# Optimization experiments

Hardware: AMD Instinct MI355X
Metric: run time of the kernel (lower is better)

## Reference

```python
import jax, jax.numpy as jnp
import numpy as np

B, H, W, C = 32, 56, 56, 256
WS = 7            # window size (hard-coded 49=7*7 in original topk modules)
NH = 8            # num heads
HD = C // NH      # head dim = 32
KCH = HD // 2     # channel top-k = 16
KSPT = 28         # spatial top-k
N = WS * WS       # 49 tokens per window
SCALE = HD ** -0.5
MLP_H = 4 * C

def _rel_index(ws):
    coords = np.stack(np.meshgrid(np.arange(ws), np.arange(ws), indexing='ij')).reshape(2, -1)
    rc = (coords[:, :, None] - coords[:, None, :]).transpose(1, 2, 0).astype(np.int64)
    rc[:, :, 0] += ws - 1
    rc[:, :, 1] += ws - 1
    rc[:, :, 0] *= 2 * ws - 1
    return jnp.asarray(rc.sum(-1))  # (N, N)

REL_IDX = _rel_index(WS)

def setup_inputs():
    key = jax.random.key(0)
    ks = jax.random.split(key, 10)
    p = lambda k, shp: jax.random.normal(k, shp, jnp.float32) * 0.02
    return dict(
        x=jax.random.normal(ks[0], (B, H * W, C), jnp.float32),
        norm1_g=jnp.ones((C,), jnp.float32), norm1_b=jnp.zeros((C,), jnp.float32),
        wq=p(ks[1], (C, C)), bq=jnp.zeros((C,), jnp.float32),
        wk=p(ks[2], (C // 2, C // 2)), bk=jnp.zeros((C // 2,), jnp.float32),
        wv=p(ks[3], (C, C)), bv=jnp.zeros((C,), jnp.float32),
        wproj=p(ks[4], (C, C)), bproj=jnp.zeros((C,), jnp.float32),
        wch=p(ks[5], (2 * HD, HD)), bch=jnp.zeros((HD,), jnp.float32),
        rpb_table=p(ks[6], ((2 * WS - 1) ** 2, NH)),
        norm2_g=jnp.ones((C,), jnp.float32), norm2_b=jnp.zeros((C,), jnp.float32),
        w1=p(ks[7], (C, MLP_H)), b1=jnp.zeros((MLP_H,), jnp.float32),
        w2=p(ks[8], (MLP_H, C)), b2=jnp.zeros((C,), jnp.float32),
    )

def _ln(x, g, b):
    mu = x.mean(-1, keepdims=True)
    var = x.var(-1, keepdims=True)
    return (x - mu) / jnp.sqrt(var + 1e-5) * g + b

def reference(x, norm1_g, norm1_b, wq, bq, wk, bk, wv, bv, wproj, bproj,
              wch, bch, rpb_table, norm2_g, norm2_b, w1, b1, w2, b2):
    shortcut = x
    xn = _ln(x, norm1_g, norm1_b).reshape(B, H, W, C)
    # window partition -> (Bw, N, C)
    xw = xn.reshape(B, H // WS, WS, W // WS, WS, C).transpose(0, 1, 3, 2, 4, 5).reshape(-1, N, C)
    Bw = xw.shape[0]
    q = xw @ wq + bq                                                    # (Bw, N, C)
    qh = q.reshape(Bw, N, NH, HD).transpose(0, 2, 1, 3).reshape(Bw * NH, N, HD)
    # ---- channel top-k (ChannelTopk) ----
    feat = jnp.concatenate([qh.mean(1), qh.max(1)], axis=-1)            # (Bn, 2*HD)
    score = jax.nn.softmax(jax.nn.gelu(feat @ wch + bch, approximate=False), axis=1)
    _, cidx = jax.lax.top_k(score, KCH)
    cidx = jnp.sort(cidx, axis=-1)                                      # sorted channel indices
    qcha = jnp.take_along_axis(qh, cidx[:, None, :], axis=2)            # (Bn, N, KCH)
    qcha1 = qcha.reshape(Bw, NH, N, KCH).transpose(0, 2, 1, 3).reshape(Bw, N, C // 2)
    k = qcha1 @ wk + bk                                                 # (Bw, N, C/2)
    # ---- relative position bias ----
    rpb = rpb_table[REL_IDX.reshape(-1)].reshape(N, N, NH).transpose(2, 0, 1)  # (NH, N, N)
    # ---- spatial top-k (SptialTopk) ----
    _, sidx = jax.lax.top_k(qh.mean(-1), KSPT)
    sidx = jnp.sort(sidx, axis=-1)                                      # (Bn, KSPT)
    qal = jnp.take_along_axis(qcha, sidx[:, :, None], axis=1)           # (Bn, KSPT, KCH)
    vsel = jnp.take_along_axis(qh, sidx[:, :, None], axis=1)            # (Bn, KSPT, HD)
    sidx_h = sidx.reshape(Bw, NH, KSPT)
    yal = jnp.take_along_axis(
        jnp.broadcast_to(rpb[None], (Bw, NH, N, N)),
        jnp.broadcast_to(sidx_h[:, :, None, :], (Bw, NH, N, KSPT)), axis=-1)  # (Bw, NH, N, KSPT)
    # ---- attention ----
    v = vsel.reshape(Bw, NH, KSPT, HD).transpose(0, 2, 1, 3).reshape(Bw, KSPT, C)
    v = (v @ wv + bv).reshape(Bw, KSPT, NH, HD).transpose(0, 2, 1, 3)   # (Bw, NH, KSPT, HD)
    qspt = (qal * SCALE).reshape(Bw, NH, KSPT, KCH)
    kh = k.reshape(Bw, N, NH, KCH).transpose(0, 2, 1, 3)                # (Bw, NH, N, KCH)
    attn = jnp.einsum('bnqc,bnkc->bnqk', kh, qspt) + yal                # (Bw, NH, N, KSPT)
    gate = jax.nn.sigmoid(attn.mean(-1))                                # (Bw, NH, N)
    attn = jax.nn.softmax(attn, axis=-1)
    o = jnp.einsum('bnqk,bnkd->bnqd', attn, v) * gate[..., None]        # (Bw, NH, N, HD)
    o = o.transpose(0, 2, 1, 3).reshape(Bw, N, C)
    o = o @ wproj + bproj
    # window reverse -> (B, L, C)
    xr = o.reshape(B, H // WS, W // WS, WS, WS, C).transpose(0, 1, 3, 2, 4, 5).reshape(B, H * W, C)
    x = shortcut + xr
    h = jax.nn.gelu(_ln(x, norm2_g, norm2_b) @ w1 + b1, approximate=False)
    return x + h @ w2 + b2
```

## Files before the change

### kernel.cpp

```cpp
#include <hip/hip_runtime.h>
#include <hip/hip_bf16.h>
#include <cmath>

#define CC 256
#define WSZ 7
#define WWD_ 56
#define NHD 8
#define HDIM 32
#define KCHN 16
#define KSP 28
#define NTOK 49
#define NWIN 2048
#define NBH 16384
#define LL 3136
#define MTOK 100352
#define MLPH 1024
#define SCALE_Q 0.17677669529663689f

typedef float floatx4 __attribute__((ext_vector_type(4)));
typedef __bf16 bf16x8_t __attribute__((ext_vector_type(8)));

__device__ __forceinline__ float gelu_f(float x) {
    return 0.5f * x * (1.0f + erff(x * 0.7071067811865475f));
}

__device__ __forceinline__ void lds_dma16(const void* g, void* l) {
    __builtin_amdgcn_global_load_lds((__attribute__((address_space(1))) void*)(void*)g,
                                     (__attribute__((address_space(3))) void*)l, 16, 0, 0);
}

__global__ __launch_bounds__(64) void ln_stats_k(const float* __restrict__ x,
                                                 float* __restrict__ mu,
                                                 float* __restrict__ rs) {
    int row = blockIdx.x;
    int lane = threadIdx.x;
    float4 v = reinterpret_cast<const float4*>(x + (size_t)row * CC)[lane];
    float s = v.x + v.y + v.z + v.w;
    float s2 = v.x * v.x + v.y * v.y + v.z * v.z + v.w * v.w;
#pragma unroll
    for (int off = 32; off > 0; off >>= 1) {
        s += __shfl_down(s, off);
        s2 += __shfl_down(s2, off);
    }
    if (lane == 0) {
        float m = s * (1.0f / CC);
        float var = s2 * (1.0f / CC) - m * m;
        mu[row] = m;
        rs[row] = rsqrtf(var + 1e-5f);
    }
}

struct GP {
    const float* W;
    const float* bias;
    float* C;
    int N, K;
    const float* x;
    const float* mu;
    const float* rs;
    const float* g;
    const float* be;
};

__global__ __launch_bounds__(256, 6) void gemm_q_k(GP p) {
    __shared__ __align__(16) float As[16][68];
    __shared__ __align__(16) float Bs[16][128];
    const int bm = blockIdx.x * 64;
    const int bn = blockIdx.y * 128;
    const int t = threadIdx.x;
    const int tx = t & 31;
    const int ty = t >> 5;
    const int w = t >> 6;

    const int ar = t >> 2;
    const int ak = (t & 3) * 4;

    const int r = bm + ar;
    int bwi = r / NTOK, n = r - bwi * NTOK;
    int b = bwi >> 6, rem = bwi & 63;
    int hw = rem >> 3, ww = rem & 7;
    int i0 = n / WSZ, j0 = n - i0 * WSZ;
    size_t grow = (size_t)b * LL + (size_t)(hw * WSZ + i0) * WWD_ + (ww * WSZ + j0);
    const float m = p.mu[grow], rsg = p.rs[grow];
    const float* xrow = p.x + grow * CC + ak;
    const float* gl = p.g + ak;
    const float* bl = p.be + ak;

    float acc[8][4] = {};

    for (int k0 = 0; k0 < CC; k0 += 16) {
        {
            float4 xv = *reinterpret_cast<const float4*>(xrow + k0);
            float4 gv = *reinterpret_cast<const float4*>(gl + k0);
            float4 bv = *reinterpret_cast<const float4*>(bl + k0);
            As[ak + 0][ar] = (xv.x - m) * rsg * gv.x + bv.x;
            As[ak + 1][ar] = (xv.y - m) * rsg * gv.y + bv.y;
            As[ak + 2][ar] = (xv.z - m) * rsg * gv.z + bv.z;
            As[ak + 3][ar] = (xv.w - m) * rsg * gv.w + bv.w;
        }
#pragma unroll
        for (int j = 0; j < 2; ++j) {
            const int c = j * 256 + t;
            const float* gp = p.W + (size_t)(k0 + (c >> 5)) * CC + bn + (c & 31) * 4;
            lds_dma16(gp, (char*)&Bs[0][0] + j * 4096 + w * 1024);
        }
        __syncthreads();
#pragma unroll
        for (int kk = 0; kk < 16; ++kk) {
            float a[8], bb[4];
            *(float4*)&a[0] = *(const float4*)&As[kk][ty * 8];
            *(float4*)&a[4] = *(const float4*)&As[kk][ty * 8 + 4];
            *(float4*)&bb[0] = *(const float4*)&Bs[kk][tx * 4];
#pragma unroll
            for (int i = 0; i < 8; ++i)
#pragma unroll
                for (int j = 0; j < 4; ++j) acc[i][j] = fmaf(a[i], bb[j], acc[i][j]);
        }
        __syncthreads();
    }

    float bj[4];
#pragma unroll
    for (int j = 0; j < 4; ++j) bj[j] = p.bias[bn + tx * 4 + j];
#pragma unroll
    for (int i = 0; i < 8; ++i) {
        const int row = bm + ty * 8 + i;
        float4 o = {acc[i][0] + bj[0], acc[i][1] + bj[1], acc[i][2] + bj[2], acc[i][3] + bj[3]};
        *reinterpret_cast<float4*>(p.C + (size_t)row * CC + bn + tx * 4) = o;
    }
}

struct MG {
    const __hip_bfloat16* A;
    const __hip_bfloat16* B;
    const float* bias;
    int N, K;
    float* Cf;
    __hip_bfloat16* Cb;
    const float* resid;
    int row0;
};

template <int EPI>
__global__ __launch_bounds__(256) void mgemm_k(MG p) {
    __shared__ __align__(16) __hip_bfloat16 As[2][128 * 32];
    __shared__ __align__(16) __hip_bfloat16 Bs[2][128 * 32];
    const int bm = blockIdx.x * 128;
    const int bn = blockIdx.y * 128;
    const int t = threadIdx.x;
    const int lane = t & 63;
    const int w = t >> 6;
    const int wm = (w & 1) * 64;
    const int wn = (w >> 1) * 64;
    const int fr = lane & 15;
    const int fk = (lane >> 4) * 8;

    const int m0 = t >> 2, m1 = (t + 256) >> 2;
    const int kc = (t & 3) * 8;
    const __hip_bfloat16* a0 = p.A + (size_t)(bm + m0) * p.K + kc;
    const __hip_bfloat16* a1 = p.A + (size_t)(bm + m1) * p.K + kc;
    const __hip_bfloat16* b0 = p.B + (size_t)(bn + m0) * p.K + kc;
    const __hip_bfloat16* b1 = p.B + (size_t)(bn + m1) * p.K + kc;

    auto stage = [&](int buf, int k0) {
        lds_dma16(a0 + k0, &As[buf][w * 512]);
        lds_dma16(a1 + k0, &As[buf][2048 + w * 512]);
        lds_dma16(b0 + k0, &Bs[buf][w * 512]);
        lds_dma16(b1 + k0, &Bs[buf][2048 + w * 512]);
    };

    floatx4 acc[4][4] = {};

    stage(0, 0);
    __syncthreads();
    int cur = 0;
    for (int k0 = 0; k0 < p.K; k0 += 32) {
        if (k0 + 32 < p.K) stage(cur ^ 1, k0 + 32);
        bf16x8_t af[4], bf[4];
#pragma unroll
        for (int i = 0; i < 4; ++i)
            af[i] = *(const bf16x8_t*)&As[cur][(wm + i * 16 + fr) * 32 + fk];
#pragma unroll
        for (int j = 0; j < 4; ++j)
            bf[j] = *(const bf16x8_t*)&Bs[cur][(wn + j * 16 + fr) * 32 + fk];
#pragma unroll
        for (int i = 0; i < 4; ++i)
#pragma unroll
            for (int j = 0; j < 4; ++j)
                acc[i][j] = __builtin_amdgcn_mfma_f32_16x16x32_bf16(af[i], bf[j], acc[i][j], 0, 0, 0);
        __syncthreads();
        cur ^= 1;
    }

    float bj[4];
#pragma unroll
    for (int j = 0; j < 4; ++j) bj[j] = p.bias[bn + wn + j * 16 + fr];
#pragma unroll
    for (int i = 0; i < 4; ++i) {
#pragma unroll
        for (int r = 0; r < 4; ++r) {
            const int m = bm + wm + i * 16 + (lane >> 4) * 4 + r;
#pragma unroll
            for (int j = 0; j < 4; ++j) {
                const int n = bn + wn + j * 16 + fr;
                float v = acc[i][j][r] + bj[j];
                if constexpr (EPI == 0) {
                    p.Cb[(size_t)m * p.N + n] = __float2bfloat16(v);
                } else if constexpr (EPI == 1) {
                    int bwi = m / NTOK, nn = m - bwi * NTOK;
                    int b = bwi >> 6, rem = bwi & 63;
                    int hw = rem >> 3, wwp = rem & 7;
                    int ii = nn / WSZ, jj = nn - ii * WSZ;
                    size_t oidx = ((size_t)b * LL + (size_t)(hw * WSZ + ii) * WWD_ + (wwp * WSZ + jj)) * CC + n;
                    p.Cf[oidx] = v + p.resid[oidx];
                } else if constexpr (EPI == 2) {
                    p.Cb[(size_t)m * p.N + n] = __float2bfloat16(gelu_f(v));
                } else {
                    size_t gr = (size_t)(m + p.row0);
                    p.Cf[gr * p.N + n] = v + p.resid[gr * p.N + n];
                }
            }
        }
    }
}

__global__ __launch_bounds__(256) void wt_k(const float* __restrict__ W,
                                            __hip_bfloat16* __restrict__ Wt, int K, int N) {
    int g = blockIdx.x * 256 + threadIdx.x;
    if (g >= K * N) return;
    int n = g / K, kk = g - n * K;
    Wt[g] = __float2bfloat16(W[(size_t)kk * N + n]);
}

__global__ __launch_bounds__(64) void topk_k(const float* __restrict__ q,
                                             const float* __restrict__ wch,
                                             const float* __restrict__ bch,
                                             short* __restrict__ cidx,
                                             short* __restrict__ sidx) {
    int bnh = blockIdx.x;
    int bwi = bnh >> 3, h = bnh & 7;
    int lane = threadIdx.x;
    __shared__ float tile[NTOK][HDIM + 1];
    __shared__ float feat[2 * HDIM];
    __shared__ float score[HDIM];
    __shared__ float rowm[NTOK];
    const float* qbase = q + ((size_t)bwi * NTOK) * CC + h * HDIM;
    for (int idx = lane; idx < NTOK * HDIM; idx += 64) {
        int n = idx >> 5, d = idx & 31;
        tile[n][d] = qbase[(size_t)n * CC + d];
    }
    __syncthreads();
    if (lane < HDIM) {
        float s = 0.f, mx = -INFINITY;
        for (int n = 0; n < NTOK; ++n) {
            float v = tile[n][lane];
            s += v;
            mx = fmaxf(mx, v);
        }
        feat[lane] = s * (1.0f / NTOK);
        feat[HDIM + lane] = mx;
    }
    if (lane < NTOK) {
        float s = 0.f;
        for (int d = 0; d < HDIM; ++d) s += tile[lane][d];
        rowm[lane] = s;
    }
    __syncthreads();
    if (lane < HDIM) {
        float s = bch[lane];
        for (int j = 0; j < 2 * HDIM; ++j) s += feat[j] * wch[j * HDIM + lane];
        score[lane] = gelu_f(s);
    }
    __syncthreads();
    {
        bool sel = false;
        if (lane < HDIM) {
            float sv = score[lane];
            int rank = 0;
            for (int j = 0; j < HDIM; ++j) {
                float oj = score[j];
                rank += (oj > sv) || (oj == sv && j < lane);
            }
            sel = rank < KCHN;
        }
        unsigned long long m = __ballot(sel);
        if (sel) {
            int pos = __popcll(m & ((1ull << lane) - 1ull));
            cidx[(size_t)bnh * KCHN + pos] = (short)lane;
        }
    }
    {
        bool sel = false;
        if (lane < NTOK) {
            float sv = rowm[lane];
            int rank = 0;
            for (int j = 0; j < NTOK; ++j) {
                float oj = rowm[j];
                rank += (oj > sv) || (oj == sv && j < lane);
            }
            sel = rank < KSP;
        }
        unsigned long long m = __ballot(sel);
        if (sel) {
            int pos = __popcll(m & ((1ull << lane) - 1ull));
            sidx[(size_t)bnh * KSP + pos] = (short)lane;
        }
    }
}

__global__ __launch_bounds__(256) void gather_ch_k(const float* __restrict__ q,
                                                   const short* __restrict__ cidx,
                                                   __hip_bfloat16* __restrict__ ak) {
    int g = blockIdx.x * 256 + threadIdx.x;
    int r = g >> 7, kk = g & 127;
    int bwi = r / NTOK;
    int hp = kk >> 4, c = kk & 15;
    int ci = cidx[((size_t)(bwi * NHD + hp)) * KCHN + c];
    ak[g] = __float2bfloat16(q[(size_t)r * CC + hp * HDIM + ci]);
}

__global__ __launch_bounds__(256) void gather_sp_k(const float* __restrict__ q,
                                                   const short* __restrict__ sidx,
                                                   __hip_bfloat16* __restrict__ av) {
    int g = blockIdx.x * 256 + threadIdx.x;
    int rr = g >> 8, c = g & 255;
    int bwi = rr / KSP, s = rr - bwi * KSP;
    int tok = sidx[((size_t)(bwi * NHD + (c >> 5))) * KSP + s];
    av[g] = __float2bfloat16(q[((size_t)(bwi * NTOK + tok)) * CC + c]);
}

__global__ __launch_bounds__(512) void attn_k(const float* __restrict__ q,
                                              const __hip_bfloat16* __restrict__ kb,
                                              const __hip_bfloat16* __restrict__ vb,
                                              const short* __restrict__ cidx,
                                              const short* __restrict__ sidx,
                                              const float* __restrict__ rpb,
                                              __hip_bfloat16* __restrict__ ob) {
    const int bwi = blockIdx.x;
    const int tid = threadIdx.x;
    const int h = tid >> 6;
    const int lane = tid & 63;
    __shared__ __hip_bfloat16 kh_s[NTOK][132];
    __shared__ float v_s[KSP][256];
    __shared__ float qs_s[NHD][KSP][KCHN];
    __shared__ int sidx_s[NHD][KSP];
    __shared__ int cidx_s[NHD][KCHN];

    if (tid < NHD * KSP) {
        sidx_s[tid / KSP][tid % KSP] = sidx[(size_t)bwi * NHD * KSP + tid];
    } else if (tid < NHD * KSP + NHD * KCHN) {
        int u = tid - NHD * KSP;
        cidx_s[u / KCHN][u % KCHN] = cidx[(size_t)bwi * NHD * KCHN + u];
    }
    {
        const __hip_bfloat16* kbase = kb + (size_t)bwi * NTOK * (NHD * KCHN);
        for (int ch = tid; ch < NTOK * 16; ch += 512) {
            int n = ch >> 4, c8 = (ch & 15) * 8;
            uint4 u = *(const uint4*)(kbase + n * 128 + c8);
            uint2* dst = (uint2*)&kh_s[n][c8];
            dst[0] = make_uint2(u.x, u.y);
            dst[1] = make_uint2(u.z, u.w);
        }
    }
    {
        const __hip_bfloat16* vbase = vb + (size_t)bwi * KSP * CC;
        for (int ch = tid; ch < KSP * 32; ch += 512) {
            int n = ch >> 5, c8 = (ch & 31) * 8;
            union { uint4 u; __hip_bfloat16 b[8]; } tt;
            tt.u = *(const uint4*)(vbase + n * CC + c8);
#pragma unroll
            for (int j = 0; j < 8; ++j) v_s[n][c8 + j] = __bfloat162float(tt.b[j]);
        }
    }
    __syncthreads();
#pragma unroll
    for (int k = 0; k < 7; ++k) {
        int idx = tid + k * 512;
        int hh = idx / (KSP * KCHN), r = idx - hh * (KSP * KCHN);
        int s = r >> 4, c = r & 15;
        qs_s[hh][s][c] =
            q[((size_t)bwi * NTOK + sidx_s[hh][s]) * CC + hh * HDIM + cidx_s[hh][c]] * SCALE_Q;
    }
    __syncthreads();

    if (lane < NTOK) {
        float khr[16];
        {
            const uint* kp = (const uint*)&kh_s[lane][h * KCHN];
#pragma unroll
            for (int j = 0; j < 8; ++j) {
                uint u = kp[j];
                __hip_bfloat162 b2 = *(__hip_bfloat162*)&u;
                float2 f = __bfloat1622float2(b2);
                khr[2 * j] = f.x;
                khr[2 * j + 1] = f.y;
            }
        }
        int i1 = lane / WSZ, j1 = lane - i1 * WSZ;
        float a[KSP];
        float msum = 0.f;
#pragma unroll
        for (int s = 0; s < KSP; ++s) {
            const float* qrow = &qs_s[h][s][0];
            float dot = 0.f;
#pragma unroll
            for (int c = 0; c < KCHN; ++c) dot += khr[c] * qrow[c];
            int m = sidx_s[h][s];
            int i2 = m / WSZ, j2 = m - i2 * WSZ;
            float bias = rpb[(size_t)((i1 - i2 + 6) * 13 + (j1 - j2 + 6)) * NHD + h];
            a[s] = dot + bias;
            msum += a[s];
        }
        float gate = 1.0f / (1.0f + expf(-msum * (1.0f / KSP)));
        float mx = -INFINITY;
#pragma unroll
        for (int s = 0; s < KSP; ++s) mx = fmaxf(mx, a[s]);
        float sum = 0.f;
#pragma unroll
        for (int s = 0; s < KSP; ++s) {
            a[s] = expf(a[s] - mx);
            sum += a[s];
        }
        float inv = gate / sum;
        float4 ov[8];
#pragma unroll
        for (int d4 = 0; d4 < 8; ++d4) ov[d4] = float4{0.f, 0.f, 0.f, 0.f};
#pragma unroll
        for (int s = 0; s < KSP; ++s) {
            const float4* vrow = (const float4*)&v_s[s][h * HDIM];
            float as = a[s];
#pragma unroll
            for (int d4 = 0; d4 < 8; ++d4) {
                float4 vv = vrow[d4];
                ov[d4].x += as * vv.x;
                ov[d4].y += as * vv.y;
                ov[d4].z += as * vv.z;
                ov[d4].w += as * vv.w;
            }
        }
        __hip_bfloat16* orow = ob + ((size_t)bwi * NTOK + lane) * CC + h * HDIM;
#pragma unroll
        for (int d4 = 0; d4 < 8; ++d4) {
            union { __hip_bfloat16 b[4]; uint2 u; } pk;
            pk.b[0] = __float2bfloat16(ov[d4].x * inv);
            pk.b[1] = __float2bfloat16(ov[d4].y * inv);
            pk.b[2] = __float2bfloat16(ov[d4].z * inv);
            pk.b[3] = __float2bfloat16(ov[d4].w * inv);
            *(uint2*)(orow + d4 * 4) = pk.u;
        }
    }
}

__global__ __launch_bounds__(64) void ln2_k(const float* __restrict__ x2,
                                            const float* __restrict__ g,
                                            const float* __restrict__ b,
                                            __hip_bfloat16* __restrict__ a2) {
    int row = blockIdx.x;
    int lane = threadIdx.x;
    float4 v = reinterpret_cast<const float4*>(x2 + (size_t)row * CC)[lane];
    float s = v.x + v.y + v.z + v.w;
    float s2 = v.x * v.x + v.y * v.y + v.z * v.z + v.w * v.w;
#pragma unroll
    for (int off = 1; off < 64; off <<= 1) {
        s += __shfl_xor(s, off);
        s2 += __shfl_xor(s2, off);
    }
    float m = s * (1.0f / CC);
    float rsg = rsqrtf(s2 * (1.0f / CC) - m * m + 1e-5f);
    float4 gv = reinterpret_cast<const float4*>(g)[lane];
    float4 bv = reinterpret_cast<const float4*>(b)[lane];
    __hip_bfloat16* orow = a2 + (size_t)row * CC + lane * 4;
    orow[0] = __float2bfloat16((v.x - m) * rsg * gv.x + bv.x);
    orow[1] = __float2bfloat16((v.y - m) * rsg * gv.y + bv.y);
    orow[2] = __float2bfloat16((v.z - m) * rsg * gv.z + bv.z);
    orow[3] = __float2bfloat16((v.w - m) * rsg * gv.w + bv.w);
}

extern "C" void kernel_launch(void* const* d_in, const int* in_sizes, int n_in,
                              void* d_out, int out_size, void* d_ws, size_t ws_size,
                              hipStream_t stream) {
    const float* x   = (const float*)d_in[0];
    const float* n1g = (const float*)d_in[1];
    const float* n1b = (const float*)d_in[2];
    const float* wq  = (const float*)d_in[3];
    const float* bq  = (const float*)d_in[4];
    const float* wk  = (const float*)d_in[5];
    const float* bk  = (const float*)d_in[6];
    const float* wv  = (const float*)d_in[7];
    const float* bv  = (const float*)d_in[8];
    const float* wpj = (const float*)d_in[9];
    const float* bpj = (const float*)d_in[10];
    const float* wch = (const float*)d_in[11];
    const float* bch = (const float*)d_in[12];
    const float* rpb = (const float*)d_in[13];
    const float* n2g = (const float*)d_in[14];
    const float* n2b = (const float*)d_in[15];
    const float* w1  = (const float*)d_in[16];
    const float* b1  = (const float*)d_in[17];
    const float* w2  = (const float*)d_in[18];
    const float* b2  = (const float*)d_in[19];
    float* out = (float*)d_out;

    char* wsb = (char*)d_ws;
    float* qb            = (float*)wsb;
    __hip_bfloat16* g1   = (__hip_bfloat16*)(wsb + 102760448);
    __hip_bfloat16* g2   = (__hip_bfloat16*)(wsb + 128450560);
    __hip_bfloat16* ob   = g1;
    __hip_bfloat16* kb   = (__hip_bfloat16*)(wsb + 157810688);
    __hip_bfloat16* vb   = (__hip_bfloat16*)(wsb + 183500800);
    float* mu1           = (float*)(wsb + 212860928);
    float* rs1           = mu1 + MTOK;
    short* cidx          = (short*)(wsb + 213663744);
    short* sidx          = (short*)(wsb + 214188032);
    __hip_bfloat16* wkt  = (__hip_bfloat16*)(wsb + 215105536);
    __hip_bfloat16* wvt  = (__hip_bfloat16*)(wsb + 215138304);
    __hip_bfloat16* wpt  = (__hip_bfloat16*)(wsb + 215269376);
    __hip_bfloat16* w1t  = (__hip_bfloat16*)(wsb + 215400448);
    __hip_bfloat16* w2t  = (__hip_bfloat16*)(wsb + 215924736);
    __hip_bfloat16* a2   = (__hip_bfloat16*)qb;
    __hip_bfloat16* hb   = (__hip_bfloat16*)(wsb + 102760448);
    if (ws_size < 216449024ULL) return;

    wt_k<<<(128 * 128 + 255) / 256, 256, 0, stream>>>(wk, wkt, 128, 128);
    wt_k<<<(256 * 256 + 255) / 256, 256, 0, stream>>>(wv, wvt, 256, 256);
    wt_k<<<(256 * 256 + 255) / 256, 256, 0, stream>>>(wpj, wpt, 256, 256);
    wt_k<<<(256 * 1024 + 255) / 256, 256, 0, stream>>>(w1, w1t, 256, 1024);
    wt_k<<<(1024 * 256 + 255) / 256, 256, 0, stream>>>(w2, w2t, 1024, 256);

    ln_stats_k<<<MTOK, 64, 0, stream>>>(x, mu1, rs1);

    GP p{};
    p.W = wq; p.bias = bq; p.C = qb; p.N = CC; p.K = CC;
    p.x = x; p.mu = mu1; p.rs = rs1; p.g = n1g; p.be = n1b;
    gemm_q_k<<<dim3(MTOK / 64, 2), 256, 0, stream>>>(p);

    topk_k<<<NBH, 64, 0, stream>>>(qb, wch, bch, cidx, sidx);

    gather_ch_k<<<MTOK * 128 / 256, 256, 0, stream>>>(qb, cidx, g1);
    MG m{};
    m.A = g1; m.B = wkt; m.bias = bk; m.N = 128; m.K = 128; m.Cb = kb;
    mgemm_k<0><<<dim3(MTOK / 128, 1), 256, 0, stream>>>(m);

    gather_sp_k<<<NWIN * KSP * 256 / 256, 256, 0, stream>>>(qb, sidx, g2);
    m = MG{};
    m.A = g2; m.B = wvt; m.bias = bv; m.N = CC; m.K = CC; m.Cb = vb;
    mgemm_k<0><<<dim3(NWIN * KSP / 128, 2), 256, 0, stream>>>(m);

    attn_k<<<NWIN, 512, 0, stream>>>(qb, kb, vb, cidx, sidx, rpb, ob);

    m = MG{};
    m.A = ob; m.B = wpt; m.bias = bpj; m.N = CC; m.K = CC; m.Cf = out; m.resid = x;
    mgemm_k<1><<<dim3(MTOK / 128, 2), 256, 0, stream>>>(m);

    ln2_k<<<MTOK, 64, 0, stream>>>(out, n2g, n2b, a2);

    const int CHUNK = MTOK / 2;
    for (int c = 0; c < 2; ++c) {
        int start = c * CHUNK;
        m = MG{};
        m.A = a2 + (size_t)start * CC; m.B = w1t; m.bias = b1;
        m.N = MLPH; m.K = CC; m.Cb = hb;
        mgemm_k<2><<<dim3(CHUNK / 128, MLPH / 128), 256, 0, stream>>>(m);

        m = MG{};
        m.A = hb; m.B = w2t; m.bias = b2; m.N = CC; m.K = MLPH;
        m.Cf = out; m.resid = out; m.row0 = start;
        mgemm_k<3><<<dim3(CHUNK / 128, CC / 128), 256, 0, stream>>>(m);
    }
}
```

Baseline: 1.051 ms.

## Precompute windowed LayerNorm output and reorder GEMM block rasterization by column-fastest

The stats-only LayerNorm kernel is replaced by one that writes the full normalized, window-partitioned activations to a scratch buffer. The Q GEMM then reads contiguous rows instead of gathering and normalizing scattered rows inside its loop. All matrix-core GEMMs now use a 1D grid where the N-tile index varies fastest, so blocks sharing an A tile run together and can reuse it in cache. The cost is an extra ~100MB write and read of normalized activations.

```diff
diff --git a/kernel.cpp b/kernel.cpp
--- a/kernel.cpp
+++ b/kernel.cpp
@@ -29,37 +29,39 @@
                                      (__attribute__((address_space(3))) void*)l, 16, 0, 0);
 }
 
-__global__ __launch_bounds__(64) void ln_stats_k(const float* __restrict__ x,
-                                                 float* __restrict__ mu,
-                                                 float* __restrict__ rs) {
-    int row = blockIdx.x;
+__global__ __launch_bounds__(64) void xn_k(const float* __restrict__ x,
+                                           const float* __restrict__ g,
+                                           const float* __restrict__ be,
+                                           float* __restrict__ xn) {
+    int r = blockIdx.x;
     int lane = threadIdx.x;
-    float4 v = reinterpret_cast<const float4*>(x + (size_t)row * CC)[lane];
+    int bwi = r / NTOK, n = r - bwi * NTOK;
+    int b = bwi >> 6, rem = bwi & 63;
+    int hw = rem >> 3, ww = rem & 7;
+    int i0 = n / WSZ, j0 = n - i0 * WSZ;
+    size_t grow = (size_t)b * LL + (size_t)(hw * WSZ + i0) * WWD_ + (ww * WSZ + j0);
+    float4 v = reinterpret_cast<const float4*>(x + grow * CC)[lane];
     float s = v.x + v.y + v.z + v.w;
     float s2 = v.x * v.x + v.y * v.y + v.z * v.z + v.w * v.w;
 #pragma unroll
-    for (int off = 32; off > 0; off >>= 1) {
-        s += __shfl_down(s, off);
-        s2 += __shfl_down(s2, off);
-    }
-    if (lane == 0) {
-        float m = s * (1.0f / CC);
-        float var = s2 * (1.0f / CC) - m * m;
-        mu[row] = m;
-        rs[row] = rsqrtf(var + 1e-5f);
-    }
+    for (int off = 1; off < 64; off <<= 1) {
+        s += __shfl_xor(s, off);
+        s2 += __shfl_xor(s2, off);
+    }
+    float m = s * (1.0f / CC);
+    float rsg = rsqrtf(s2 * (1.0f / CC) - m * m + 1e-5f);
+    float4 gv = reinterpret_cast<const float4*>(g)[lane];
+    float4 bv = reinterpret_cast<const float4*>(be)[lane];
+    float4 o = {(v.x - m) * rsg * gv.x + bv.x, (v.y - m) * rsg * gv.y + bv.y,
+                (v.z - m) * rsg * gv.z + bv.z, (v.w - m) * rsg * gv.w + bv.w};
+    reinterpret_cast<float4*>(xn + (size_t)r * CC)[lane] = o;
 }
 
 struct GP {
     const float* W;
     const float* bias;
     float* C;
-    int N, K;
-    const float* x;
-    const float* mu;
-    const float* rs;
-    const float* g;
-    const float* be;
+    const float* xn;
 };
 
 __global__ __launch_bounds__(256, 6) void gemm_q_k(GP p) {
@@ -74,34 +76,22 @@
 
     const int ar = t >> 2;
     const int ak = (t & 3) * 4;
-
-    const int r = bm + ar;
-    int bwi = r / NTOK, n = r - bwi * NTOK;
-    int b = bwi >> 6, rem = bwi & 63;
-    int hw = rem >> 3, ww = rem & 7;
-    int i0 = n / WSZ, j0 = n - i0 * WSZ;
-    size_t grow = (size_t)b * LL + (size_t)(hw * WSZ + i0) * WWD_ + (ww * WSZ + j0);
-    const float m = p.mu[grow], rsg = p.rs[grow];
-    const float* xrow = p.x + grow * CC + ak;
-    const float* gl = p.g + ak;
-    const float* bl = p.be + ak;
+    const float* arow = p.xn + (size_t)(bm + ar) * CC + ak;
 
     float acc[8][4] = {};
 
     for (int k0 = 0; k0 < CC; k0 += 16) {
         {
-            float4 xv = *reinterpret_cast<const float4*>(xrow + k0);
-            float4 gv = *reinterpret_cast<const float4*>(gl + k0);
-            float4 bv = *reinterpret_cast<const float4*>(bl + k0);
-            As[ak + 0][ar] = (xv.x - m) * rsg * gv.x + bv.x;
-            As[ak + 1][ar] = (xv.y - m) * rsg * gv.y + bv.y;
-            As[ak + 2][ar] = (xv.z - m) * rsg * gv.z + bv.z;
-            As[ak + 3][ar] = (xv.w - m) * rsg * gv.w + bv.w;
+            float4 xv = *reinterpret_cast<const float4*>(arow + k0);
+            As[ak + 0][ar] = xv.x;
+            As[ak + 1][ar] = xv.y;
+            As[ak + 2][ar] = xv.z;
+            As[ak + 3][ar] = xv.w;
         }
 #pragma unroll
         for (int j = 0; j < 2; ++j) {
             const int c = j * 256 + t;
-            const float* gp = p.W + (size_t)(k0 + (c >> 5)) * CC + bn + (c & 31) * 4;
+            const float* gp = p.W + (size_t)((c >> 5) + k0) * CC + bn + (c & 31) * 4;
             lds_dma16(gp, (char*)&Bs[0][0] + j * 4096 + w * 1024);
         }
         __syncthreads();
@@ -139,14 +129,16 @@
     __hip_bfloat16* Cb;
     const float* resid;
     int row0;
+    int gy;
 };
 
 template <int EPI>
 __global__ __launch_bounds__(256) void mgemm_k(MG p) {
     __shared__ __align__(16) __hip_bfloat16 As[2][128 * 32];
     __shared__ __align__(16) __hip_bfloat16 Bs[2][128 * 32];
-    const int bm = blockIdx.x * 128;
-    const int bn = blockIdx.y * 128;
+    const int bid = blockIdx.x;
+    const int bm = (bid / p.gy) * 128;
+    const int bn = (bid % p.gy) * 128;
     const int t = threadIdx.x;
     const int lane = t & 63;
     const int w = t >> 6;
@@ -503,13 +495,12 @@
 
     char* wsb = (char*)d_ws;
     float* qb            = (float*)wsb;
+    float* xn            = (float*)(wsb + 102760448);
     __hip_bfloat16* g1   = (__hip_bfloat16*)(wsb + 102760448);
     __hip_bfloat16* g2   = (__hip_bfloat16*)(wsb + 128450560);
     __hip_bfloat16* ob   = g1;
     __hip_bfloat16* kb   = (__hip_bfloat16*)(wsb + 157810688);
     __hip_bfloat16* vb   = (__hip_bfloat16*)(wsb + 183500800);
-    float* mu1           = (float*)(wsb + 212860928);
-    float* rs1           = mu1 + MTOK;
     short* cidx          = (short*)(wsb + 213663744);
     short* sidx          = (short*)(wsb + 214188032);
     __hip_bfloat16* wkt  = (__hip_bfloat16*)(wsb + 215105536);
@@ -527,30 +518,29 @@
     wt_k<<<(256 * 1024 + 255) / 256, 256, 0, stream>>>(w1, w1t, 256, 1024);
     wt_k<<<(1024 * 256 + 255) / 256, 256, 0, stream>>>(w2, w2t, 1024, 256);
 
-    ln_stats_k<<<MTOK, 64, 0, stream>>>(x, mu1, rs1);
+    xn_k<<<MTOK, 64, 0, stream>>>(x, n1g, n1b, xn);
 
     GP p{};
-    p.W = wq; p.bias = bq; p.C = qb; p.N = CC; p.K = CC;
-    p.x = x; p.mu = mu1; p.rs = rs1; p.g = n1g; p.be = n1b;
+    p.W = wq; p.bias = bq; p.C = qb; p.xn = xn;
     gemm_q_k<<<dim3(MTOK / 64, 2), 256, 0, stream>>>(p);
 
     topk_k<<<NBH, 64, 0, stream>>>(qb, wch, bch, cidx, sidx);
 
     gather_ch_k<<<MTOK * 128 / 256, 256, 0, stream>>>(qb, cidx, g1);
     MG m{};
-    m.A = g1; m.B = wkt; m.bias = bk; m.N = 128; m.K = 128; m.Cb = kb;
-    mgemm_k<0><<<dim3(MTOK / 128, 1), 256, 0, stream>>>(m);
+    m.A = g1; m.B = wkt; m.bias = bk; m.N = 128; m.K = 128; m.Cb = kb; m.gy = 1;
+    mgemm_k<0><<<MTOK / 128, 256, 0, stream>>>(m);
 
     gather_sp_k<<<NWIN * KSP * 256 / 256, 256, 0, stream>>>(qb, sidx, g2);
     m = MG{};
-    m.A = g2; m.B = wvt; m.bias = bv; m.N = CC; m.K = CC; m.Cb = vb;
-    mgemm_k<0><<<dim3(NWIN * KSP / 128, 2), 256, 0, stream>>>(m);
+    m.A = g2; m.B = wvt; m.bias = bv; m.N = CC; m.K = CC; m.Cb = vb; m.gy = 2;
+    mgemm_k<0><<<(NWIN * KSP / 128) * 2, 256, 0, stream>>>(m);
 
     attn_k<<<NWIN, 512, 0, stream>>>(qb, kb, vb, cidx, sidx, rpb, ob);
 
     m = MG{};
-    m.A = ob; m.B = wpt; m.bias = bpj; m.N = CC; m.K = CC; m.Cf = out; m.resid = x;
-    mgemm_k<1><<<dim3(MTOK / 128, 2), 256, 0, stream>>>(m);
+    m.A = ob; m.B = wpt; m.bias = bpj; m.N = CC; m.K = CC; m.Cf = out; m.resid = x; m.gy = 2;
+    mgemm_k<1><<<(MTOK / 128) * 2, 256, 0, stream>>>(m);
 
     ln2_k<<<MTOK, 64, 0, stream>>>(out, n2g, n2b, a2);
 
@@ -559,12 +549,12 @@
         int start = c * CHUNK;
         m = MG{};
         m.A = a2 + (size_t)start * CC; m.B = w1t; m.bias = b1;
-        m.N = MLPH; m.K = CC; m.Cb = hb;
-        mgemm_k<2><<<dim3(CHUNK / 128, MLPH / 128), 256, 0, stream>>>(m);
+        m.N = MLPH; m.K = CC; m.Cb = hb; m.gy = MLPH / 128;
+        mgemm_k<2><<<(CHUNK / 128) * (MLPH / 128), 256, 0, stream>>>(m);
 
         m = MG{};
         m.A = hb; m.B = w2t; m.bias = b2; m.N = CC; m.K = MLPH;
-        m.Cf = out; m.resid = out; m.row0 = start;
-        mgemm_k<3><<<dim3(CHUNK / 128, CC / 128), 256, 0, stream>>>(m);
-    }
-}
+        m.Cf = out; m.resid = out; m.row0 = start; m.gy = 2;
+        mgemm_k<3><<<(CHUNK / 128) * 2, 256, 0, stream>>>(m);
+    }
+}
```

Result: no change. 1.060 ms (+0.9%).

## Widen Q GEMM tile to full N and linearize MFMA GEMM grid with N-fastest order

Applied to the files above, without the earlier changes.

The fp32 Q projection kernel now computes all 256 output columns per block, so the fused LayerNorm'd A tile is built once instead of twice, and each thread accumulates an 8x8 tile. The bf16 MFMA GEMM moves to a 1D grid where consecutive blocks share the same A row tile across N tiles, which should improve L2 reuse of A. The larger Q tile raises register and LDS use, and the launch bound drops to 4 blocks per CU, lowering occupancy.

```diff
diff --git a/kernel.cpp b/kernel.cpp
--- a/kernel.cpp
+++ b/kernel.cpp
@@ -54,7 +54,6 @@
     const float* W;
     const float* bias;
     float* C;
-    int N, K;
     const float* x;
     const float* mu;
     const float* rs;
@@ -62,11 +61,10 @@
     const float* be;
 };
 
-__global__ __launch_bounds__(256, 6) void gemm_q_k(GP p) {
+__global__ __launch_bounds__(256, 4) void gemm_q_k(GP p) {
     __shared__ __align__(16) float As[16][68];
-    __shared__ __align__(16) float Bs[16][128];
+    __shared__ __align__(16) float Bs[16][256];
     const int bm = blockIdx.x * 64;
-    const int bn = blockIdx.y * 128;
     const int t = threadIdx.x;
     const int tx = t & 31;
     const int ty = t >> 5;
@@ -86,7 +84,7 @@
     const float* gl = p.g + ak;
     const float* bl = p.be + ak;
 
-    float acc[8][4] = {};
+    float acc[8][8] = {};
 
     for (int k0 = 0; k0 < CC; k0 += 16) {
         {
@@ -99,34 +97,41 @@
             As[ak + 3][ar] = (xv.w - m) * rsg * gv.w + bv.w;
         }
 #pragma unroll
-        for (int j = 0; j < 2; ++j) {
+        for (int j = 0; j < 4; ++j) {
             const int c = j * 256 + t;
-            const float* gp = p.W + (size_t)(k0 + (c >> 5)) * CC + bn + (c & 31) * 4;
+            const float* gp = p.W + (size_t)(k0 + (c >> 6)) * CC + (c & 63) * 4;
             lds_dma16(gp, (char*)&Bs[0][0] + j * 4096 + w * 1024);
         }
         __syncthreads();
 #pragma unroll
         for (int kk = 0; kk < 16; ++kk) {
-            float a[8], bb[4];
+            float a[8], bb[8];
             *(float4*)&a[0] = *(const float4*)&As[kk][ty * 8];
             *(float4*)&a[4] = *(const float4*)&As[kk][ty * 8 + 4];
             *(float4*)&bb[0] = *(const float4*)&Bs[kk][tx * 4];
+            *(float4*)&bb[4] = *(const float4*)&Bs[kk][128 + tx * 4];
 #pragma unroll
             for (int i = 0; i < 8; ++i)
 #pragma unroll
-                for (int j = 0; j < 4; ++j) acc[i][j] = fmaf(a[i], bb[j], acc[i][j]);
+                for (int j = 0; j < 8; ++j) acc[i][j] = fmaf(a[i], bb[j], acc[i][j]);
         }
         __syncthreads();
     }
 
-    float bj[4];
-#pragma unroll
-    for (int j = 0; j < 4; ++j) bj[j] = p.bias[bn + tx * 4 + j];
+    float bj0[4], bj1[4];
+#pragma unroll
+    for (int j = 0; j < 4; ++j) {
+        bj0[j] = p.bias[tx * 4 + j];
+        bj1[j] = p.bias[128 + tx * 4 + j];
+    }
 #pragma unroll
     for (int i = 0; i < 8; ++i) {
         const int row = bm + ty * 8 + i;
-        float4 o = {acc[i][0] + bj[0], acc[i][1] + bj[1], acc[i][2] + bj[2], acc[i][3] + bj[3]};
-        *reinterpret_cast<float4*>(p.C + (size_t)row * CC + bn + tx * 4) = o;
+        float* crow = p.C + (size_t)row * CC;
+        float4 o0 = {acc[i][0] + bj0[0], acc[i][1] + bj0[1], acc[i][2] + bj0[2], acc[i][3] + bj0[3]};
+        float4 o1 = {acc[i][4] + bj1[0], acc[i][5] + bj1[1], acc[i][6] + bj1[2], acc[i][7] + bj1[3]};
+        *reinterpret_cast<float4*>(crow + tx * 4) = o0;
+        *reinterpret_cast<float4*>(crow + 128 + tx * 4) = o1;
     }
 }
 
@@ -139,14 +144,16 @@
     __hip_bfloat16* Cb;
     const float* resid;
     int row0;
+    int gy;
 };
 
 template <int EPI>
 __global__ __launch_bounds__(256) void mgemm_k(MG p) {
     __shared__ __align__(16) __hip_bfloat16 As[2][128 * 32];
     __shared__ __align__(16) __hip_bfloat16 Bs[2][128 * 32];
-    const int bm = blockIdx.x * 128;
-    const int bn = blockIdx.y * 128;
+    const int bid = blockIdx.x;
+    const int bm = (bid / p.gy) * 128;
+    const int bn = (bid % p.gy) * 128;
     const int t = threadIdx.x;
     const int lane = t & 63;
     const int w = t >> 6;
@@ -530,27 +537,27 @@
     ln_stats_k<<<MTOK, 64, 0, stream>>>(x, mu1, rs1);
 
     GP p{};
-    p.W = wq; p.bias = bq; p.C = qb; p.N = CC; p.K = CC;
+    p.W = wq; p.bias = bq; p.C = qb;
     p.x = x; p.mu = mu1; p.rs = rs1; p.g = n1g; p.be = n1b;
-    gemm_q_k<<<dim3(MTOK / 64, 2), 256, 0, stream>>>(p);
+    gemm_q_k<<<dim3(MTOK / 64), 256, 0, stream>>>(p);
 
     topk_k<<<NBH, 64, 0, stream>>>(qb, wch, bch, cidx, sidx);
 
     gather_ch_k<<<MTOK * 128 / 256, 256, 0, stream>>>(qb, cidx, g1);
     MG m{};
-    m.A = g1; m.B = wkt; m.bias = bk; m.N = 128; m.K = 128; m.Cb = kb;
-    mgemm_k<0><<<dim3(MTOK / 128, 1), 256, 0, stream>>>(m);
+    m.A = g1; m.B = wkt; m.bias = bk; m.N = 128; m.K = 128; m.Cb = kb; m.gy = 1;
+    mgemm_k<0><<<MTOK / 128, 256, 0, stream>>>(m);
 
     gather_sp_k<<<NWIN * KSP * 256 / 256, 256, 0, stream>>>(qb, sidx, g2);
     m = MG{};
-    m.A = g2; m.B = wvt; m.bias = bv; m.N = CC; m.K = CC; m.Cb = vb;
-    mgemm_k<0><<<dim3(NWIN * KSP / 128, 2), 256, 0, stream>>>(m);
+    m.A = g2; m.B = wvt; m.bias = bv; m.N = CC; m.K = CC; m.Cb = vb; m.gy = 2;
+    mgemm_k<0><<<(NWIN * KSP / 128) * 2, 256, 0, stream>>>(m);
 
     attn_k<<<NWIN, 512, 0, stream>>>(qb, kb, vb, cidx, sidx, rpb, ob);
 
     m = MG{};
-    m.A = ob; m.B = wpt; m.bias = bpj; m.N = CC; m.K = CC; m.Cf = out; m.resid = x;
-    mgemm_k<1><<<dim3(MTOK / 128, 2), 256, 0, stream>>>(m);
+    m.A = ob; m.B = wpt; m.bias = bpj; m.N = CC; m.K = CC; m.Cf = out; m.resid = x; m.gy = 2;
+    mgemm_k<1><<<(MTOK / 128) * 2, 256, 0, stream>>>(m);
 
     ln2_k<<<MTOK, 64, 0, stream>>>(out, n2g, n2b, a2);
 
@@ -559,12 +566,12 @@
         int start = c * CHUNK;
         m = MG{};
         m.A = a2 + (size_t)start * CC; m.B = w1t; m.bias = b1;
-        m.N = MLPH; m.K = CC; m.Cb = hb;
-        mgemm_k<2><<<dim3(CHUNK / 128, MLPH / 128), 256, 0, stream>>>(m);
+        m.N = MLPH; m.K = CC; m.Cb = hb; m.gy = MLPH / 128;
+        mgemm_k<2><<<(CHUNK / 128) * (MLPH / 128), 256, 0, stream>>>(m);
 
         m = MG{};
         m.A = hb; m.B = w2t; m.bias = b2; m.N = CC; m.K = MLPH;
-        m.Cf = out; m.resid = out; m.row0 = start;
-        mgemm_k<3><<<dim3(CHUNK / 128, CC / 128), 256, 0, stream>>>(m);
-    }
-}
+        m.Cf = out; m.resid = out; m.row0 = start; m.gy = 2;
+        mgemm_k<3><<<(CHUNK / 128) * 2, 256, 0, stream>>>(m);
+    }
+}
```

New measurement: 1.048 ms. No clear change (-0.2%).
